# Optimization experiments

Hardware: AMD Instinct MI355X
Metric: run time of the kernel (lower is better)

The kernel has to match this reference:

```python
import jax, jax.numpy as jnp
import numpy as np

N = 100000
D = 128          # atom_input_dim
OUT = 256        # output_dim
HOPS = 3
E = 640000
IN_DIM = D * (HOPS + 1)  # 512


def setup_inputs() -> dict:
    key = jax.random.key(0)
    ks = jax.random.split(key, 16)
    s = 0.02
    inp = {
        "x": jax.random.normal(ks[0], (N, D), dtype=jnp.float32),
        "target": jax.random.randint(ks[1], (E,), 0, HOPS * N, dtype=jnp.int64),
        "src": jax.random.randint(ks[2], (E,), 0, HOPS * N, dtype=jnp.int64),
        "W_in": jax.random.normal(ks[3], (IN_DIM, OUT), dtype=jnp.float32) * s,
        "b_in": jnp.zeros((OUT,), dtype=jnp.float32),
        "W1_0": jax.random.normal(ks[4], (OUT, OUT), dtype=jnp.float32) * s,
        "b1_0": jnp.zeros((OUT,), dtype=jnp.float32),
        "W2_0": jax.random.normal(ks[5], (OUT, OUT), dtype=jnp.float32) * s,
        "b2_0": jnp.zeros((OUT,), dtype=jnp.float32),
        "W1_1": jax.random.normal(ks[6], (OUT, OUT), dtype=jnp.float32) * s,
        "b1_1": jnp.zeros((OUT,), dtype=jnp.float32),
        "W2_1": jax.random.normal(ks[7], (OUT, OUT), dtype=jnp.float32) * s,
        "b2_1": jnp.zeros((OUT,), dtype=jnp.float32),
        "W_skip": jax.random.normal(ks[8], (IN_DIM, OUT), dtype=jnp.float32) * s,
        "b_skip": jnp.zeros((OUT,), dtype=jnp.float32),
    }
    return inp


def reference(x, target, src, W_in, b_in, W1_0, b1_0, W2_0, b2_0,
              W1_1, b1_1, W2_1, b2_1, W_skip, b_skip):
    n = x.shape[0]
    # multi-hop message passing: tile node features HOPS times, gather by src,
    # scatter-add into target over the tiled index space [0, HOPS*n)
    expanded = jnp.tile(x, (HOPS, 1))                       # [HOPS*n, D]
    agg = jnp.zeros_like(expanded).at[target].add(expanded[src])
    # split per-hop chunks and concat with original features -> [n, (HOPS+1)*D]
    feats = jnp.concatenate([x] + [agg[h * n:(h + 1) * n] for h in range(HOPS)], axis=-1)
    h = jax.nn.silu(feats @ W_in + b_in)                    # [n, OUT]
    global_skip = feats @ W_skip + b_skip                   # input_dim != output_dim
    for W1, b1, W2, b2 in ((W1_0, b1_0, W2_0, b2_0), (W1_1, b1_1, W2_1, b2_1)):
        h = (jax.nn.silu(h @ W1 + b1)) @ W2 + b2 + h        # residual MLP block (dropout=0)
    return h + global_skip
```

## Files before the change

kernel.cpp:

```cpp
#include <hip/hip_runtime.h>
#include <math.h>

#define NN 100000
#define DD 128
#define OUT_DIM 256
#define HOPS 3
#define EDGES 640000
#define TGT (HOPS*NN)

typedef short bf16x8 __attribute__((ext_vector_type(8)));
typedef float f32x4 __attribute__((ext_vector_type(4)));

__device__ __forceinline__ unsigned short f2bf(float f) {
    unsigned u = __float_as_uint(f);
    unsigned r = u + 0x7FFFu + ((u >> 16) & 1u);
    return (unsigned short)(r >> 16);
}
__device__ __forceinline__ float bf2f(unsigned short s) {
    return __uint_as_float(((unsigned)s) << 16);
}
__device__ __forceinline__ float silu(float v) { return v / (1.0f + expf(-v)); }

__device__ __forceinline__ int swz(int c, int r) {
    return (c & ~63) | ((c & 63) ^ ((r & 7) << 3));
}

__device__ __forceinline__ void gload16(const unsigned short* g, unsigned short* l) {
    __builtin_amdgcn_global_load_lds(
        (const __attribute__((address_space(1))) void*)g,
        (__attribute__((address_space(3))) void*)l, 16, 0, 0);
}

__global__ __launch_bounds__(256) void k_hist(const int* __restrict__ tgt,
                                              int* __restrict__ cnt) {
    int e = blockIdx.x * 256 + threadIdx.x;
    atomicAdd(&cnt[tgt[e]], 1);
}

__global__ __launch_bounds__(512) void k_scanb(const int* __restrict__ cnt,
                                               int* __restrict__ off,
                                               int* __restrict__ part, int n) {
    __shared__ int s[512];
    int tid = threadIdx.x;
    int g = blockIdx.x * 512 + tid;
    int v = (g < n) ? cnt[g] : 0;
    s[tid] = v;
    __syncthreads();
    for (int d = 1; d < 512; d <<= 1) {
        int a = (tid >= d) ? s[tid - d] : 0;
        __syncthreads();
        s[tid] += a;
        __syncthreads();
    }
    if (g < n) off[g] = s[tid] - v;
    if (tid == 511) part[blockIdx.x] = s[511];
}

__global__ __launch_bounds__(1024) void k_scanp(int* __restrict__ part, int n) {
    __shared__ int s[1024];
    int t = threadIdx.x;
    s[t] = (t < n) ? part[t] : 0;
    __syncthreads();
    for (int d = 1; d < 1024; d <<= 1) {
        int a = (t >= d) ? s[t - d] : 0;
        __syncthreads();
        s[t] += a;
        __syncthreads();
    }
    if (t < n) part[t] = s[t];
}

__global__ __launch_bounds__(512) void k_addoff(int* __restrict__ off,
                                                const int* __restrict__ part,
                                                int* __restrict__ cursor, int n) {
    int g = blockIdx.x * 512 + threadIdx.x;
    if (g >= n) return;
    int add = (blockIdx.x > 0) ? part[blockIdx.x - 1] : 0;
    int o = off[g] + add;
    off[g] = o;
    cursor[g] = o;
}

__global__ __launch_bounds__(256) void k_fill(const int* __restrict__ tgt,
                                              const int* __restrict__ src,
                                              int* __restrict__ cursor,
                                              int* __restrict__ esrc) {
    int e = blockIdx.x * 256 + threadIdx.x;
    int t = tgt[e];
    int p = atomicAdd(&cursor[t], 1);
    esrc[p] = src[e] % NN;
}

__global__ __launch_bounds__(256) void k_aggfeats(const float* __restrict__ x,
                                                  const int* __restrict__ off,
                                                  const int* __restrict__ cur,
                                                  const int* __restrict__ esrc,
                                                  unsigned* __restrict__ feats) {
    int lane = threadIdx.x & 63;
    int r = blockIdx.x * 4 + (threadIdx.x >> 6);
    const float2* x2 = (const float2*)x;
    if (r < NN) {
        float2 v = x2[(size_t)r * 64 + lane];
        int p = lane;
        int ps = (p & ~31) | ((p & 31) ^ ((r & 7) << 2));
        feats[(size_t)r * 256 + ps] =
            (unsigned)f2bf(v.x) | ((unsigned)f2bf(v.y) << 16);
    } else {
        int t = r - NN;
        int hop = t / NN;
        int tn = t - hop * NN;
        int b = off[t], e = cur[t];
        float ax = 0.f, ay = 0.f;
        for (int i = b; i < e; ++i) {
            int sn = esrc[i];
            float2 v = x2[(size_t)sn * 64 + lane];
            ax += v.x; ay += v.y;
        }
        int p = 64 + hop * 64 + lane;
        int ps = (p & ~31) | ((p & 31) ^ ((tn & 7) << 2));
        feats[(size_t)tn * 256 + ps] =
            (unsigned)f2bf(ax) | ((unsigned)f2bf(ay) << 16);
    }
}

__global__ __launch_bounds__(256) void k_wprep(
    const float* __restrict__ Win, const float* __restrict__ Wskip,
    const float* __restrict__ W10, const float* __restrict__ W20,
    const float* __restrict__ W11, const float* __restrict__ W21,
    unsigned short* __restrict__ Wt1, unsigned short* __restrict__ Wt25) {
    int idx = blockIdx.x * 256 + threadIdx.x;
    if (idx < 262144) {
        int c = idx >> 9, k = idx & 511;
        int kl = swz(k, c);
        float v = (c < 256) ? Win[kl * 256 + c] : Wskip[kl * 256 + (c - 256)];
        Wt1[idx] = f2bf(v);
    } else {
        int j = idx - 262144;
        int m = j >> 16, rr = j & 65535;
        int c = rr >> 8, k = rr & 255;
        int kl = swz(k, c);
        const float* Wm = (m == 0) ? W10 : (m == 1) ? W20 : (m == 2) ? W11 : W21;
        Wt25[(size_t)m * 65536 + c * 256 + k] = f2bf(Wm[kl * 256 + c]);
    }
}

__global__ __launch_bounds__(256) void k_gemm1(
    const unsigned short* __restrict__ A, const unsigned short* __restrict__ Wt,
    const float* __restrict__ bias0, const float* __restrict__ bias1,
    unsigned short* __restrict__ h0, unsigned short* __restrict__ gsk) {
    const int K = 512;
    __shared__ unsigned short As[2][128 * 64];
    __shared__ unsigned short Bs[2][128 * 64];

    const int tid = threadIdx.x;
    const int lane = tid & 63;
    const int w = tid >> 6;
    const int row0 = blockIdx.x * 128;
    const int col0 = blockIdx.y * 128;

    const int wr = (w >> 1) * 64;
    const int wc = (w & 1) * 64;
    const int lr = lane & 15;
    const int lk8 = (lane >> 4) * 8;

    f32x4 acc[4][4];
    #pragma unroll
    for (int m = 0; m < 4; ++m)
        #pragma unroll
        for (int n = 0; n < 4; ++n) acc[m][n] = (f32x4){0.f, 0.f, 0.f, 0.f};

    auto STAGE = [&](int buf, int k0) {
        #pragma unroll
        for (int i = 0; i < 4; ++i) {
            int chunk = i * 4 + w;
            int slot = chunk * 64 + lane;
            int r = slot >> 3;
            int kq = (slot & 7) * 8;
            gload16(A + (size_t)(row0 + r) * K + k0 + kq, &As[buf][chunk * 512]);
            gload16(Wt + (size_t)(col0 + r) * K + k0 + kq, &Bs[buf][chunk * 512]);
        }
    };

    STAGE(0, 0);
    asm volatile("s_waitcnt vmcnt(0)" ::: "memory");
    __syncthreads();

    for (int ks = 0; ks < 8; ++ks) {
        int cur = ks & 1;
        if (ks + 1 < 8) STAGE(cur ^ 1, (ks + 1) * 64);

        #pragma unroll
        for (int ks2 = 0; ks2 < 2; ++ks2) {
            bf16x8 af[4], bfr[4];
            #pragma unroll
            for (int m = 0; m < 4; ++m) {
                int row = wr + m * 16 + lr;
                int eo = (ks2 * 32 + lk8) ^ ((row & 7) << 3);
                af[m] = *(const bf16x8*)&As[cur][row * 64 + eo];
            }
            #pragma unroll
            for (int n = 0; n < 4; ++n) {
                int row = wc + n * 16 + lr;
                int eo = (ks2 * 32 + lk8) ^ ((row & 7) << 3);
                bfr[n] = *(const bf16x8*)&Bs[cur][row * 64 + eo];
            }
            #pragma unroll
            for (int m = 0; m < 4; ++m)
                #pragma unroll
                for (int n = 0; n < 4; ++n)
                    acc[m][n] = __builtin_amdgcn_mfma_f32_16x16x32_bf16(
                        af[m], bfr[n], acc[m][n], 0, 0, 0);
        }
        asm volatile("s_waitcnt vmcnt(0)" ::: "memory");
        __syncthreads();
    }

    const int rq = (lane >> 4) * 4;
    #pragma unroll
    for (int m = 0; m < 4; ++m) {
        #pragma unroll
        for (int n = 0; n < 4; ++n) {
            int cg = col0 + wc + n * 16 + lr;
            float bb = (cg < OUT_DIM) ? bias0[cg] : bias1[cg - OUT_DIM];
            #pragma unroll
            for (int j = 0; j < 4; ++j) {
                int r = row0 + wr + m * 16 + rq + j;
                if (r >= NN) continue;
                float v = acc[m][n][j] + bb;
                if (cg < OUT_DIM)
                    h0[(size_t)r * OUT_DIM + swz(cg, r)] = f2bf(silu(v));
                else
                    gsk[(size_t)r * OUT_DIM + (cg - OUT_DIM)] = f2bf(v);
            }
        }
    }
}

template <int FINAL>
__global__ __launch_bounds__(512) void k_mlp(
    const unsigned short* __restrict__ Hin,
    const unsigned short* __restrict__ W1t, const unsigned short* __restrict__ W2t,
    const float* __restrict__ b1, const float* __restrict__ b2,
    const unsigned short* __restrict__ gsk,
    unsigned short* __restrict__ Hout, float* __restrict__ outf) {
    __shared__ unsigned short Hs[128 * 256];
    __shared__ unsigned short Ws[2][256 * 64];

    const int tid = threadIdx.x;
    const int lane = tid & 63;
    const int w = tid >> 6;
    const int wr = (w >> 1) * 32;
    const int wc = (w & 1) * 128;
    const int lr = lane & 15;
    const int lk8 = (lane >> 4) * 8;
    const int row0 = blockIdx.x * 128;

    auto STAGE_W = [&](const unsigned short* Wt, int buf, int ks) {
        #pragma unroll
        for (int i = 0; i < 4; ++i) {
            int chunk = w * 4 + i;
            int col = chunk * 8 + (lane >> 3);
            int ko = ks * 64 + (lane & 7) * 8;
            gload16(Wt + (size_t)col * 256 + ko, &Ws[buf][chunk * 512]);
        }
    };

    #pragma unroll
    for (int i = 0; i < 8; ++i) {
        int chunk = w * 8 + i;
        gload16(Hin + (size_t)row0 * 256 + chunk * 512 + lane * 8,
                &Hs[chunk * 512]);
    }
    STAGE_W(W1t, 0, 0);
    asm volatile("s_waitcnt vmcnt(0)" ::: "memory");
    __syncthreads();

    f32x4 acc_t[2][8];
    #pragma unroll
    for (int m = 0; m < 2; ++m)
        #pragma unroll
        for (int n = 0; n < 8; ++n) acc_t[m][n] = (f32x4){0.f, 0.f, 0.f, 0.f};

    for (int ks = 0; ks < 4; ++ks) {
        if (ks < 3) STAGE_W(W1t, (ks + 1) & 1, ks + 1);
        else        STAGE_W(W2t, 0, 0);
        #pragma unroll
        for (int ks2 = 0; ks2 < 2; ++ks2) {
            bf16x8 af[2], bfr[8];
            #pragma unroll
            for (int m = 0; m < 2; ++m) {
                int row = wr + m * 16 + lr;
                int eo = (ks2 * 32 + lk8) ^ ((row & 7) << 3);
                af[m] = *(const bf16x8*)&Hs[row * 256 + ks * 64 + eo];
            }
            #pragma unroll
            for (int n = 0; n < 8; ++n) {
                int col = wc + n * 16 + lr;
                int eo = (ks2 * 32 + lk8) ^ ((col & 7) << 3);
                bfr[n] = *(const bf16x8*)&Ws[ks & 1][col * 64 + eo];
            }
            #pragma unroll
            for (int m = 0; m < 2; ++m)
                #pragma unroll
                for (int n = 0; n < 8; ++n)
                    acc_t[m][n] = __builtin_amdgcn_mfma_f32_16x16x32_bf16(
                        af[m], bfr[n], acc_t[m][n], 0, 0, 0);
        }
        asm volatile("s_waitcnt vmcnt(0)" ::: "memory");
        __syncthreads();
    }

    const int rq = (lane >> 4) * 4;
    f32x4 acc2[2][8];
    #pragma unroll
    for (int m = 0; m < 2; ++m)
        #pragma unroll
        for (int n = 0; n < 8; ++n) {
            int col = wc + n * 16 + lr;
            float bb = b2[col];
            #pragma unroll
            for (int j = 0; j < 4; ++j) {
                int row = wr + m * 16 + rq + j;
                int sc = (col & ~63) | ((col & 63) ^ ((row & 7) << 3));
                acc2[m][n][j] = bf2f(Hs[row * 256 + sc]) + bb;
            }
        }
    __syncthreads();

    #pragma unroll
    for (int m = 0; m < 2; ++m)
        #pragma unroll
        for (int n = 0; n < 8; ++n) {
            int col = wc + n * 16 + lr;
            float bb = b1[col];
            #pragma unroll
            for (int j = 0; j < 4; ++j) {
                int row = wr + m * 16 + rq + j;
                int sc = (col & ~63) | ((col & 63) ^ ((row & 7) << 3));
                Hs[row * 256 + sc] = f2bf(silu(acc_t[m][n][j] + bb));
            }
        }
    __syncthreads();

    for (int ks = 0; ks < 4; ++ks) {
        if (ks < 3) STAGE_W(W2t, (ks + 1) & 1, ks + 1);
        #pragma unroll
        for (int ks2 = 0; ks2 < 2; ++ks2) {
            bf16x8 af[2], bfr[8];
            #pragma unroll
            for (int m = 0; m < 2; ++m) {
                int row = wr + m * 16 + lr;
                int eo = (ks2 * 32 + lk8) ^ ((row & 7) << 3);
                af[m] = *(const bf16x8*)&Hs[row * 256 + ks * 64 + eo];
            }
            #pragma unroll
            for (int n = 0; n < 8; ++n) {
                int col = wc + n * 16 + lr;
                int eo = (ks2 * 32 + lk8) ^ ((col & 7) << 3);
                bfr[n] = *(const bf16x8*)&Ws[ks & 1][col * 64 + eo];
            }
            #pragma unroll
            for (int m = 0; m < 2; ++m)
                #pragma unroll
                for (int n = 0; n < 8; ++n)
                    acc2[m][n] = __builtin_amdgcn_mfma_f32_16x16x32_bf16(
                        af[m], bfr[n], acc2[m][n], 0, 0, 0);
        }
        asm volatile("s_waitcnt vmcnt(0)" ::: "memory");
        __syncthreads();
    }

    #pragma unroll
    for (int m = 0; m < 2; ++m)
        #pragma unroll
        for (int n = 0; n < 8; ++n) {
            int col = wc + n * 16 + lr;
            #pragma unroll
            for (int j = 0; j < 4; ++j) {
                int row = wr + m * 16 + rq + j;
                int r = row0 + row;
                if (r >= NN) continue;
                if (FINAL == 0) {
                    Hout[(size_t)r * 256 + swz(col, row)] = f2bf(acc2[m][n][j]);
                } else {
                    size_t o = (size_t)r * 256 + col;
                    outf[o] = acc2[m][n][j] + bf2f(gsk[o]);
                }
            }
        }
}

extern "C" void kernel_launch(void* const* d_in, const int* in_sizes, int n_in,
                              void* d_out, int out_size, void* d_ws, size_t ws_size,
                              hipStream_t stream) {
    const float* x      = (const float*)d_in[0];
    const int*   target = (const int*)d_in[1];
    const int*   src    = (const int*)d_in[2];
    const float* W_in   = (const float*)d_in[3];
    const float* b_in   = (const float*)d_in[4];
    const float* W1_0   = (const float*)d_in[5];
    const float* b1_0   = (const float*)d_in[6];
    const float* W2_0   = (const float*)d_in[7];
    const float* b2_0   = (const float*)d_in[8];
    const float* W1_1   = (const float*)d_in[9];
    const float* b1_1   = (const float*)d_in[10];
    const float* W2_1   = (const float*)d_in[11];
    const float* b2_1   = (const float*)d_in[12];
    const float* W_skip = (const float*)d_in[13];
    const float* b_skip = (const float*)d_in[14];
    float* out = (float*)d_out;

    char* p = (char*)d_ws;
    unsigned short* feats = (unsigned short*)p; p += (size_t)NN * 512 * 2;
    unsigned short* h0    = (unsigned short*)p; p += (size_t)NN * 256 * 2;
    unsigned short* h1    = (unsigned short*)p; p += (size_t)NN * 256 * 2;
    unsigned short* gsk   = (unsigned short*)p; p += (size_t)NN * 256 * 2;
    unsigned short* Wt1   = (unsigned short*)p; p += 512 * 512 * 2;
    unsigned short* Wt25  = (unsigned short*)p; p += 4 * 256 * 256 * 2;
    int* cnt    = (int*)p; p += (size_t)TGT * 4;
    int* off    = (int*)p; p += (size_t)TGT * 4;
    int* cursor = (int*)p; p += (size_t)TGT * 4;
    int* esrc   = (int*)p; p += (size_t)EDGES * 4;
    int* part   = (int*)p; p += 4096;

    const int SCAN_BLOCKS = (TGT + 511) / 512;

    hipMemsetAsync(cnt, 0, (size_t)TGT * 4, stream);
    k_hist<<<EDGES / 256, 256, 0, stream>>>(target, cnt);
    k_scanb<<<SCAN_BLOCKS, 512, 0, stream>>>(cnt, off, part, TGT);
    k_scanp<<<1, 1024, 0, stream>>>(part, SCAN_BLOCKS);
    k_addoff<<<SCAN_BLOCKS, 512, 0, stream>>>(off, part, cursor, TGT);
    k_fill<<<EDGES / 256, 256, 0, stream>>>(target, src, cursor, esrc);

    k_aggfeats<<<NN, 256, 0, stream>>>(x, off, cursor, esrc, (unsigned*)feats);

    k_wprep<<<2048, 256, 0, stream>>>(W_in, W_skip, W1_0, W2_0, W1_1, W2_1,
                                      Wt1, Wt25);

    const int GM = (NN + 127) / 128;

    k_gemm1<<<dim3(GM, 4), 256, 0, stream>>>(feats, Wt1, b_in, b_skip, h0, gsk);

    k_mlp<0><<<GM, 512, 0, stream>>>(h0, Wt25 + 0 * 65536, Wt25 + 1 * 65536,
                                     b1_0, b2_0, nullptr, h1, nullptr);
    k_mlp<1><<<GM, 512, 0, stream>>>(h1, Wt25 + 2 * 65536, Wt25 + 3 * 65536,
                                     b1_1, b2_1, gsk, nullptr, out);
}
```

Measured before the change: 696.9 us.

## Load GEMM1 A tiles to registers and shrink MLP LDS with prepacked weights

In k_gemm1 the A operand is now read straight from global memory into registers, double-buffered, and only the weights go through LDS. This halves LDS use and launch bounds ask for 3 blocks per CU. In k_mlp the weights are prepacked in k_wprep into an MFMA-fragment order and staged one 32-wide k-slice at a time through a small 16KB LDS buffer via register prefetch. The residual is reread from global memory at the end rather than kept in registers, which lowers LDS use to allow more resident blocks. The cost is more barriers per k-step, uncoalesced-ish direct global A loads, and extra global reads for the residual.

```diff
diff --git a/kernel.cpp b/kernel.cpp
--- a/kernel.cpp
+++ b/kernel.cpp
@@ -136,20 +136,22 @@
         Wt1[idx] = f2bf(v);
     } else {
         int j = idx - 262144;
-        int m = j >> 16, rr = j & 65535;
-        int c = rr >> 8, k = rr & 255;
-        int kl = swz(k, c);
+        int m = j >> 16, r = j & 65535;
+        int tk = r >> 13;
+        int o  = (r >> 11) & 3;
+        int col = (r >> 3) & 255;
+        int e  = r & 7;
+        int k  = tk * 32 + o * 8 + e;
         const float* Wm = (m == 0) ? W10 : (m == 1) ? W20 : (m == 2) ? W11 : W21;
-        Wt25[(size_t)m * 65536 + c * 256 + k] = f2bf(Wm[kl * 256 + c]);
-    }
-}
-
-__global__ __launch_bounds__(256) void k_gemm1(
+        Wt25[(size_t)m * 65536 + r] = f2bf(Wm[k * 256 + col]);
+    }
+}
+
+__global__ __launch_bounds__(256, 3) void k_gemm1(
     const unsigned short* __restrict__ A, const unsigned short* __restrict__ Wt,
     const float* __restrict__ bias0, const float* __restrict__ bias1,
     unsigned short* __restrict__ h0, unsigned short* __restrict__ gsk) {
     const int K = 512;
-    __shared__ unsigned short As[2][128 * 64];
     __shared__ unsigned short Bs[2][128 * 64];
 
     const int tid = threadIdx.x;
@@ -169,39 +171,50 @@
         #pragma unroll
         for (int n = 0; n < 4; ++n) acc[m][n] = (f32x4){0.f, 0.f, 0.f, 0.f};
 
-    auto STAGE = [&](int buf, int k0) {
+    auto STAGE_B = [&](int buf, int k0) {
         #pragma unroll
         for (int i = 0; i < 4; ++i) {
             int chunk = i * 4 + w;
             int slot = chunk * 64 + lane;
             int r = slot >> 3;
             int kq = (slot & 7) * 8;
-            gload16(A + (size_t)(row0 + r) * K + k0 + kq, &As[buf][chunk * 512]);
             gload16(Wt + (size_t)(col0 + r) * K + k0 + kq, &Bs[buf][chunk * 512]);
         }
     };
 
-    STAGE(0, 0);
+    bf16x8 a[2][4][2];
+    auto LOAD_A = [&](int buf, int ks) {
+        #pragma unroll
+        for (int m = 0; m < 4; ++m) {
+            int row = row0 + wr + m * 16 + lr;
+            #pragma unroll
+            for (int k2 = 0; k2 < 2; ++k2) {
+                int k = ks * 64 + k2 * 32 + lk8;
+                int eo = (k & ~63) | ((k & 63) ^ ((row & 7) << 3));
+                a[buf][m][k2] = *(const bf16x8*)(A + (size_t)row * K + eo);
+            }
+        }
+    };
+
+    LOAD_A(0, 0);
+    STAGE_B(0, 0);
     asm volatile("s_waitcnt vmcnt(0)" ::: "memory");
     __syncthreads();
 
+    #pragma unroll
     for (int ks = 0; ks < 8; ++ks) {
         int cur = ks & 1;
-        if (ks + 1 < 8) STAGE(cur ^ 1, (ks + 1) * 64);
-
-        #pragma unroll
-        for (int ks2 = 0; ks2 < 2; ++ks2) {
-            bf16x8 af[4], bfr[4];
-            #pragma unroll
-            for (int m = 0; m < 4; ++m) {
-                int row = wr + m * 16 + lr;
-                int eo = (ks2 * 32 + lk8) ^ ((row & 7) << 3);
-                af[m] = *(const bf16x8*)&As[cur][row * 64 + eo];
-            }
+        if (ks < 7) {
+            STAGE_B(cur ^ 1, (ks + 1) * 64);
+            LOAD_A(cur ^ 1, ks + 1);
+        }
+        #pragma unroll
+        for (int k2 = 0; k2 < 2; ++k2) {
+            bf16x8 bfr[4];
             #pragma unroll
             for (int n = 0; n < 4; ++n) {
                 int row = wc + n * 16 + lr;
-                int eo = (ks2 * 32 + lk8) ^ ((row & 7) << 3);
+                int eo = (k2 * 32 + lk8) ^ ((row & 7) << 3);
                 bfr[n] = *(const bf16x8*)&Bs[cur][row * 64 + eo];
             }
             #pragma unroll
@@ -209,9 +222,11 @@
                 #pragma unroll
                 for (int n = 0; n < 4; ++n)
                     acc[m][n] = __builtin_amdgcn_mfma_f32_16x16x32_bf16(
-                        af[m], bfr[n], acc[m][n], 0, 0, 0);
-        }
-        asm volatile("s_waitcnt vmcnt(0)" ::: "memory");
+                        a[cur][m][k2], bfr[n], acc[m][n], 0, 0, 0);
+        }
+        if (ks < 7) {
+            asm volatile("s_waitcnt vmcnt(8)" ::: "memory");
+        }
         __syncthreads();
     }
 
@@ -237,14 +252,14 @@
 }
 
 template <int FINAL>
-__global__ __launch_bounds__(512) void k_mlp(
+__global__ __launch_bounds__(512, 4) void k_mlp(
     const unsigned short* __restrict__ Hin,
     const unsigned short* __restrict__ W1t, const unsigned short* __restrict__ W2t,
     const float* __restrict__ b1, const float* __restrict__ b2,
     const unsigned short* __restrict__ gsk,
     unsigned short* __restrict__ Hout, float* __restrict__ outf) {
     __shared__ unsigned short Hs[128 * 256];
-    __shared__ unsigned short Ws[2][256 * 64];
+    __shared__ unsigned short Ws[8192];
 
     const int tid = threadIdx.x;
     const int lane = tid & 63;
@@ -253,80 +268,64 @@
     const int wc = (w & 1) * 128;
     const int lr = lane & 15;
     const int lk8 = (lane >> 4) * 8;
+    const int o16 = (lane >> 4) * 256;
     const int row0 = blockIdx.x * 128;
 
-    auto STAGE_W = [&](const unsigned short* Wt, int buf, int ks) {
-        #pragma unroll
-        for (int i = 0; i < 4; ++i) {
-            int chunk = w * 4 + i;
-            int col = chunk * 8 + (lane >> 3);
-            int ko = ks * 64 + (lane & 7) * 8;
-            gload16(Wt + (size_t)col * 256 + ko, &Ws[buf][chunk * 512]);
-        }
+    bf16x8 wA, wB;
+    auto LOADW = [&](int t) {
+        const unsigned short* base = ((t < 8) ? W1t : W2t) + (t & 7) * 8192;
+        wA = *(const bf16x8*)(base + tid * 16);
+        wB = *(const bf16x8*)(base + tid * 16 + 8);
+    };
+    auto PUTW = [&]() {
+        *(bf16x8*)&Ws[tid * 16] = wA;
+        *(bf16x8*)&Ws[tid * 16 + 8] = wB;
     };
 
     #pragma unroll
     for (int i = 0; i < 8; ++i) {
         int chunk = w * 8 + i;
-        gload16(Hin + (size_t)row0 * 256 + chunk * 512 + lane * 8,
-                &Hs[chunk * 512]);
-    }
-    STAGE_W(W1t, 0, 0);
+        gload16(Hin + (size_t)row0 * 256 + chunk * 512 + lane * 8, &Hs[chunk * 512]);
+    }
+    LOADW(0);
     asm volatile("s_waitcnt vmcnt(0)" ::: "memory");
     __syncthreads();
-
-    f32x4 acc_t[2][8];
+    PUTW();
+    LOADW(1);
+    __syncthreads();
+
+    f32x4 acc[2][8];
     #pragma unroll
     for (int m = 0; m < 2; ++m)
         #pragma unroll
-        for (int n = 0; n < 8; ++n) acc_t[m][n] = (f32x4){0.f, 0.f, 0.f, 0.f};
-
-    for (int ks = 0; ks < 4; ++ks) {
-        if (ks < 3) STAGE_W(W1t, (ks + 1) & 1, ks + 1);
-        else        STAGE_W(W2t, 0, 0);
-        #pragma unroll
-        for (int ks2 = 0; ks2 < 2; ++ks2) {
-            bf16x8 af[2], bfr[8];
-            #pragma unroll
-            for (int m = 0; m < 2; ++m) {
-                int row = wr + m * 16 + lr;
-                int eo = (ks2 * 32 + lk8) ^ ((row & 7) << 3);
-                af[m] = *(const bf16x8*)&Hs[row * 256 + ks * 64 + eo];
-            }
-            #pragma unroll
-            for (int n = 0; n < 8; ++n) {
-                int col = wc + n * 16 + lr;
-                int eo = (ks2 * 32 + lk8) ^ ((col & 7) << 3);
-                bfr[n] = *(const bf16x8*)&Ws[ks & 1][col * 64 + eo];
-            }
-            #pragma unroll
-            for (int m = 0; m < 2; ++m)
-                #pragma unroll
-                for (int n = 0; n < 8; ++n)
-                    acc_t[m][n] = __builtin_amdgcn_mfma_f32_16x16x32_bf16(
-                        af[m], bfr[n], acc_t[m][n], 0, 0, 0);
-        }
-        asm volatile("s_waitcnt vmcnt(0)" ::: "memory");
+        for (int n = 0; n < 8; ++n) acc[m][n] = (f32x4){0.f, 0.f, 0.f, 0.f};
+
+    #pragma unroll
+    for (int s = 0; s < 8; ++s) {
+        bf16x8 af[2], bfr[8];
+        int kk = s * 32 + lk8;
+        #pragma unroll
+        for (int m = 0; m < 2; ++m) {
+            int row = wr + m * 16 + lr;
+            int eo = (kk & ~63) | ((kk & 63) ^ ((row & 7) << 3));
+            af[m] = *(const bf16x8*)&Hs[row * 256 + eo];
+        }
+        #pragma unroll
+        for (int n = 0; n < 8; ++n)
+            bfr[n] = *(const bf16x8*)&Ws[(o16 + wc + n * 16 + lr) * 8];
+        #pragma unroll
+        for (int m = 0; m < 2; ++m)
+            #pragma unroll
+            for (int n = 0; n < 8; ++n)
+                acc[m][n] = __builtin_amdgcn_mfma_f32_16x16x32_bf16(
+                    af[m], bfr[n], acc[m][n], 0, 0, 0);
+        __syncthreads();
+        PUTW();
+        LOADW(s + 2);
         __syncthreads();
     }
 
     const int rq = (lane >> 4) * 4;
-    f32x4 acc2[2][8];
-    #pragma unroll
-    for (int m = 0; m < 2; ++m)
-        #pragma unroll
-        for (int n = 0; n < 8; ++n) {
-            int col = wc + n * 16 + lr;
-            float bb = b2[col];
-            #pragma unroll
-            for (int j = 0; j < 4; ++j) {
-                int row = wr + m * 16 + rq + j;
-                int sc = (col & ~63) | ((col & 63) ^ ((row & 7) << 3));
-                acc2[m][n][j] = bf2f(Hs[row * 256 + sc]) + bb;
-            }
-        }
-    __syncthreads();
-
     #pragma unroll
     for (int m = 0; m < 2; ++m)
         #pragma unroll
@@ -336,38 +335,43 @@
             #pragma unroll
             for (int j = 0; j < 4; ++j) {
                 int row = wr + m * 16 + rq + j;
-                int sc = (col & ~63) | ((col & 63) ^ ((row & 7) << 3));
-                Hs[row * 256 + sc] = f2bf(silu(acc_t[m][n][j] + bb));
+                Hs[row * 256 + swz(col, row)] = f2bf(silu(acc[m][n][j] + bb));
             }
         }
     __syncthreads();
-
-    for (int ks = 0; ks < 4; ++ks) {
-        if (ks < 3) STAGE_W(W2t, (ks + 1) & 1, ks + 1);
-        #pragma unroll
-        for (int ks2 = 0; ks2 < 2; ++ks2) {
-            bf16x8 af[2], bfr[8];
-            #pragma unroll
-            for (int m = 0; m < 2; ++m) {
-                int row = wr + m * 16 + lr;
-                int eo = (ks2 * 32 + lk8) ^ ((row & 7) << 3);
-                af[m] = *(const bf16x8*)&Hs[row * 256 + ks * 64 + eo];
-            }
-            #pragma unroll
-            for (int n = 0; n < 8; ++n) {
-                int col = wc + n * 16 + lr;
-                int eo = (ks2 * 32 + lk8) ^ ((col & 7) << 3);
-                bfr[n] = *(const bf16x8*)&Ws[ks & 1][col * 64 + eo];
-            }
-            #pragma unroll
-            for (int m = 0; m < 2; ++m)
-                #pragma unroll
-                for (int n = 0; n < 8; ++n)
-                    acc2[m][n] = __builtin_amdgcn_mfma_f32_16x16x32_bf16(
-                        af[m], bfr[n], acc2[m][n], 0, 0, 0);
-        }
-        asm volatile("s_waitcnt vmcnt(0)" ::: "memory");
-        __syncthreads();
+    #pragma unroll
+    for (int m = 0; m < 2; ++m)
+        #pragma unroll
+        for (int n = 0; n < 8; ++n) {
+            float bb = b2[wc + n * 16 + lr];
+            acc[m][n] = (f32x4){bb, bb, bb, bb};
+        }
+
+    #pragma unroll
+    for (int s = 0; s < 8; ++s) {
+        bf16x8 af[2], bfr[8];
+        int kk = s * 32 + lk8;
+        #pragma unroll
+        for (int m = 0; m < 2; ++m) {
+            int row = wr + m * 16 + lr;
+            int eo = (kk & ~63) | ((kk & 63) ^ ((row & 7) << 3));
+            af[m] = *(const bf16x8*)&Hs[row * 256 + eo];
+        }
+        #pragma unroll
+        for (int n = 0; n < 8; ++n)
+            bfr[n] = *(const bf16x8*)&Ws[(o16 + wc + n * 16 + lr) * 8];
+        #pragma unroll
+        for (int m = 0; m < 2; ++m)
+            #pragma unroll
+            for (int n = 0; n < 8; ++n)
+                acc[m][n] = __builtin_amdgcn_mfma_f32_16x16x32_bf16(
+                    af[m], bfr[n], acc[m][n], 0, 0, 0);
+        if (s < 7) {
+            __syncthreads();
+            PUTW();
+            if (s < 6) LOADW(s + 10);
+            __syncthreads();
+        }
     }
 
     #pragma unroll
@@ -380,11 +384,12 @@
                 int row = wr + m * 16 + rq + j;
                 int r = row0 + row;
                 if (r >= NN) continue;
+                float v = acc[m][n][j] + bf2f(Hin[(size_t)r * 256 + swz(col, row)]);
                 if (FINAL == 0) {
-                    Hout[(size_t)r * 256 + swz(col, row)] = f2bf(acc2[m][n][j]);
+                    Hout[(size_t)r * 256 + swz(col, row)] = f2bf(v);
                 } else {
-                    size_t o = (size_t)r * 256 + col;
-                    outf[o] = acc2[m][n][j] + bf2f(gsk[o]);
+                    size_t ol = (size_t)r * 256 + col;
+                    outf[ol] = v + bf2f(gsk[ol]);
                 }
             }
         }
```

Result: slower. 735.1 us (+5.5%).
